# Optimization experiments

Measured on AMD Instinct MI355X. Metric: run time of the kernel, lower is better.

Reference implementation:

```python
import jax, jax.numpy as jnp
import numpy as np

B, N, C, R = 16, 1024, 256, 8
E = 262144
NUM_SUPER = 32
EPS = 1e-5


def _ln(x, g, b):
    mu = jnp.mean(x, axis=-1, keepdims=True)
    var = jnp.var(x, axis=-1, keepdims=True)
    return (x - mu) / jnp.sqrt(var + EPS) * g + b


def setup_inputs() -> dict:
    key = jax.random.key(0)
    ks = jax.random.split(key, 20)

    def w(k, shape, fan_in):
        return (jax.random.normal(k, shape, jnp.float32) / np.sqrt(fan_in)).astype(jnp.float32)

    return dict(
        x=jax.random.normal(ks[0], (B, N, C), jnp.float32),
        batch_edge_index=jax.random.randint(ks[1], (2, E), 0, B * N),
        batch_edge_types=jax.random.randint(ks[2], (E,), 0, R),
        # cross-modal attention
        Wq=w(ks[3], (C, C), C), bq=jnp.zeros((C,), jnp.float32),
        Wk=w(ks[4], (C, C), C), bk=jnp.zeros((C,), jnp.float32),
        Wv=w(ks[5], (C, C), C), bv=jnp.zeros((C,), jnp.float32),
        Wg=w(ks[6], (2 * C, C), 2 * C), bg=jnp.zeros((C,), jnp.float32),
        ln_attn_g=jnp.ones((C,), jnp.float32), ln_attn_b=jnp.zeros((C,), jnp.float32),
        # confidence net
        Wc1=w(ks[7], (C, C // 2), C), bc1=jnp.zeros((C // 2,), jnp.float32),
        Wc2=w(ks[8], (C // 2, 1), C // 2), bc2=jnp.zeros((1,), jnp.float32),
        # feature mixer
        Wm=w(ks[9], (2 * C, C), 2 * C), bm=jnp.zeros((C,), jnp.float32),
        ln1_g=jnp.ones((C,), jnp.float32), ln1_b=jnp.zeros((C,), jnp.float32),
        # RGCN
        W_rel=w(ks[10], (R, C, C), C),
        W_root=w(ks[11], (C, C), C),
        b_rgcn=jnp.zeros((C,), jnp.float32),
        ln2_g=jnp.ones((C,), jnp.float32), ln2_b=jnp.zeros((C,), jnp.float32),
        # super class head
        Wh=w(ks[12], (C, NUM_SUPER), C), bh=jnp.zeros((NUM_SUPER,), jnp.float32),
    )


def reference(x, batch_edge_index, batch_edge_types,
              Wq, bq, Wk, bk, Wv, bv, Wg, bg, ln_attn_g, ln_attn_b,
              Wc1, bc1, Wc2, bc2, Wm, bm, ln1_g, ln1_b,
              W_rel, W_root, b_rgcn, ln2_g, ln2_b, Wh, bh):
    residual = x
    q = x @ Wq + bq
    k = x @ Wk + bk
    v = x @ Wv + bv
    attn = jax.nn.softmax(jnp.einsum('bnc,bmc->bnm', q, k) / jnp.sqrt(jnp.float32(C)), axis=-1)
    out = jnp.einsum('bnm,bmc->bnc', attn, v)
    gate = jax.nn.sigmoid(jnp.concatenate([out, residual], axis=-1) @ Wg + bg)
    validated = _ln(gate * out + (1.0 - gate) * residual, ln_attn_g, ln_attn_b)

    conf = jax.nn.sigmoid(jax.nn.relu(validated @ Wc1 + bc1) @ Wc2 + bc2)  # [B,N,1]
    weighted = validated * conf
    xm = jax.nn.relu(jnp.concatenate([x, weighted], axis=-1) @ Wm + bm)
    xn = _ln(xm, ln1_g, ln1_b).reshape(B * N, C)

    # RGCNConv (PyG defaults: mean aggregation per relation, root weight, bias)
    src, dst = batch_edge_index[0], batch_edge_index[1]
    h = jnp.einsum('nc,rcd->rnd', xn, W_rel)          # [R, B*N, C] relation-transformed nodes
    msg = h[batch_edge_types, src]                    # [E, C] per-edge gather
    seg = dst * R + batch_edge_types                  # (node, relation) segment id
    cnt = jax.ops.segment_sum(jnp.ones((E,), xn.dtype), seg, num_segments=B * N * R)
    msg = msg / jnp.maximum(cnt[seg], 1.0)[:, None]
    agg = jax.ops.segment_sum(msg, dst, num_segments=B * N)
    x_rgcn = agg + xn @ W_root + b_rgcn
    x_rgcn = jax.nn.relu(_ln(x_rgcn.reshape(B, N, C), ln2_g, ln2_b))

    denom = jnp.maximum(conf.sum(axis=1), 1e-8)       # [B,1]
    pooled = (x_rgcn * conf).sum(axis=1) / denom      # [B,C]
    return pooled @ Wh + bh                           # [B, NUM_SUPER]
```

## Files before the change

### kernel.cpp

```cpp
#include <hip/hip_runtime.h>
#include <hip/hip_bf16.h>

#define B_ 16
#define N_ 1024
#define C_ 256
#define R_ 8
#define E_ 262144
#define NS_ 32
#define BN_ (B_*N_)
#define BNC_ (BN_*C_)

typedef __hip_bfloat16 bf16;
typedef __attribute__((ext_vector_type(4))) float f32x4;
typedef __attribute__((ext_vector_type(8))) short bf16x8;

__device__ __forceinline__ float b2f(bf16 x) { return __bfloat162float(x); }
__device__ __forceinline__ bf16  f2b(float x) { return __float2bfloat16(x); }
__device__ __forceinline__ float us2f(unsigned short u) { return __uint_as_float((unsigned)u << 16); }

__device__ __forceinline__ void gload16(const void* g, void* l) {
    auto gp = (const __attribute__((address_space(1))) void*)(unsigned long long)g;
    auto lp = (__attribute__((address_space(3))) void*)(unsigned)(unsigned long long)l;
    __builtin_amdgcn_global_load_lds(gp, lp, 16, 0, 0);
}

template<int ACT>
__global__ __launch_bounds__(256) void gemm_bf16(
    const bf16* __restrict__ A, int lda, long long sA,
    const bf16* __restrict__ Bm, int ldb, long long sB,
    bf16* __restrict__ Cc, int ldc, long long sC,
    const float* __restrict__ bias, const float* __restrict__ bias2,
    const float* __restrict__ bias3, int K)
{
    __shared__ short sbuf[24576];
    const int tid = threadIdx.x;
    const int lane = tid & 63, w = tid >> 6;
    const int wr = w >> 1, wc = w & 1;

    const int gx = gridDim.x;
    const int nwg = gx * gridDim.y;
    int id = blockIdx.y * gx + blockIdx.x;
    if ((nwg & 7) == 0) { const int cpx = nwg >> 3; id = (id & 7) * cpx + (id >> 3); }
    const int bm = (id / gx) * 128, bn = (id % gx) * 128;

    const bf16* Ab = A + (size_t)blockIdx.z * sA;
    const bf16* Bb = Bm + (size_t)blockIdx.z * sB;
    bf16* Cb = Cc + (size_t)blockIdx.z * sC;

    const int rg = lane >> 2;
    const int kswz = ((lane & 3) ^ ((rg >> 1) & 3)) * 8;

    f32x4 acc[4][4];
    const f32x4 zz = {0.f, 0.f, 0.f, 0.f};
    #pragma unroll
    for (int i = 0; i < 4; ++i)
        #pragma unroll
        for (int j = 0; j < 4; ++j) acc[i][j] = zz;

    const int fr = lane & 15;
    const int fm = lane >> 4;
    const int fslot = (fm ^ ((fr >> 1) & 3)) * 8;

    const int NI = K >> 5;

#define STAGE_AB(bi, kk) do {                                                          \
    _Pragma("unroll")                                                                  \
    for (int t_ = 0; t_ < 2; ++t_) {                                                   \
        gload16(Ab + (size_t)(bm + t_*64 + w*16 + rg) * lda + (kk) + kswz,             \
                sbuf + (bi)*4096 + t_*2048 + w*512);                                   \
        gload16(Bb + (size_t)(bn + t_*64 + w*16 + rg) * ldb + (kk) + kswz,             \
                sbuf + 12288 + (bi)*4096 + t_*2048 + w*512);                           \
    } } while (0)

    STAGE_AB(0, 0);
    if (NI > 1) STAGE_AB(1, 32);
    if (NI > 2) STAGE_AB(2, 64);

    int cur = 0;
    for (int i = 0; i < NI; ++i) {
        if (i + 2 < NI)      asm volatile("s_waitcnt vmcnt(8)" ::: "memory");
        else if (i + 1 < NI) asm volatile("s_waitcnt vmcnt(4)" ::: "memory");
        else                 asm volatile("s_waitcnt vmcnt(0)" ::: "memory");
        __builtin_amdgcn_s_barrier();
        __builtin_amdgcn_sched_barrier(0);

        bf16x8 af[4], bfr[4];
        const short* Ac = sbuf + cur * 4096;
        const short* Bc = sbuf + 12288 + cur * 4096;
        #pragma unroll
        for (int ii = 0; ii < 4; ++ii)
            af[ii] = *(const bf16x8*)&Ac[(wr*64 + ii*16 + fr)*32 + fslot];
        #pragma unroll
        for (int jj = 0; jj < 4; ++jj)
            bfr[jj] = *(const bf16x8*)&Bc[(wc*64 + jj*16 + fr)*32 + fslot];

        asm volatile("s_waitcnt lgkmcnt(0)" ::: "memory");
        __builtin_amdgcn_s_barrier();
        __builtin_amdgcn_sched_barrier(0);
        if (i + 3 < NI) STAGE_AB(cur, (i + 3) * 32);

        #pragma unroll
        for (int ii = 0; ii < 4; ++ii)
            #pragma unroll
            for (int jj = 0; jj < 4; ++jj)
                acc[ii][jj] = __builtin_amdgcn_mfma_f32_16x16x32_bf16(af[ii], bfr[jj], acc[ii][jj], 0, 0, 0);
        cur = (cur == 2) ? 0 : cur + 1;
    }
#undef STAGE_AB

    __syncthreads();
    const int er = (lane >> 4) * 4, ec = lane & 15;
    #pragma unroll
    for (int half = 0; half < 2; ++half) {
        if (wr == half) {
            #pragma unroll
            for (int j = 0; j < 4; ++j) {
                const int col = bn + wc*64 + j*16 + ec;
                float bvv = 0.0f;
                if (bias) {
                    const int seg = col >> 8;
                    const float* bp = (seg == 0) ? bias : (seg == 1 ? bias2 : bias3);
                    bvv = bp[col & 255];
                }
                #pragma unroll
                for (int i = 0; i < 4; ++i) {
                    #pragma unroll
                    for (int p = 0; p < 4; ++p) {
                        float val = acc[i][j][p] + bvv;
                        if (ACT == 1) val = fmaxf(val, 0.0f);
                        if (ACT == 2) val = 1.0f / (1.0f + __expf(-val));
                        *(bf16*)&sbuf[(i*16 + er + p)*136 + wc*64 + j*16 + ec] = f2b(val);
                    }
                }
            }
        }
        __syncthreads();
        #pragma unroll
        for (int it = 0; it < 4; ++it) {
            const int ch = tid + it*256;
            const int row = ch >> 4, cp = (ch & 15) * 8;
            *(bf16x8*)&Cb[(size_t)(bm + half*64 + row) * ldc + bn + cp] =
                *(const bf16x8*)&sbuf[row*136 + cp];
        }
        __syncthreads();
    }
}

template<int ACT>
__global__ __launch_bounds__(256) void gemm64_bf16(
    const bf16* __restrict__ A, int lda, long long sA,
    const bf16* __restrict__ Bm, int ldb, long long sB,
    bf16* __restrict__ Cc, int ldc, long long sC,
    const float* __restrict__ bias, int K)
{
    __shared__ short sbuf[16384];
    const int tid = threadIdx.x;
    const int lane = tid & 63, w = tid >> 6;
    const int wr = w >> 1, wc = w & 1;

    const int gx = gridDim.x;
    const int nwg = gx * gridDim.y;
    int id = blockIdx.y * gx + blockIdx.x;
    if ((nwg & 7) == 0) { const int cpx = nwg >> 3; id = (id & 7) * cpx + (id >> 3); }
    const int bm = (id / gx) * 64, bn = (id % gx) * 64;

    const bf16* Ab = A + (size_t)blockIdx.z * sA;
    const bf16* Bb = Bm + (size_t)blockIdx.z * sB;
    bf16* Cb = Cc + (size_t)blockIdx.z * sC;

    const int rg = lane >> 2;
    const int kswz = ((lane & 3) ^ ((rg >> 1) & 3)) * 8;

    f32x4 acc[2][2];
    const f32x4 zz = {0.f, 0.f, 0.f, 0.f};
    #pragma unroll
    for (int i = 0; i < 2; ++i)
        #pragma unroll
        for (int j = 0; j < 2; ++j) acc[i][j] = zz;

    const int fr = lane & 15;
    const int fm = lane >> 4;
    const int fslot = (fm ^ ((fr >> 1) & 3)) * 8;

    const int NI = K >> 5;

#define STAGE64(bi, kk) do {                                                           \
    gload16(Ab + (size_t)(bm + w*16 + rg) * lda + (kk) + kswz,                         \
            sbuf + (bi)*2048 + w*512);                                                 \
    gload16(Bb + (size_t)(bn + w*16 + rg) * ldb + (kk) + kswz,                         \
            sbuf + 8192 + (bi)*2048 + w*512);                                          \
    } while (0)

    STAGE64(0, 0);
    if (NI > 1) STAGE64(1, 32);
    if (NI > 2) STAGE64(2, 64);
    if (NI > 3) STAGE64(3, 96);

    for (int i = 0; i < NI; ++i) {
        const int cur = i & 3;
        if (i + 3 < NI)      asm volatile("s_waitcnt vmcnt(6)" ::: "memory");
        else if (i + 2 < NI) asm volatile("s_waitcnt vmcnt(4)" ::: "memory");
        else if (i + 1 < NI) asm volatile("s_waitcnt vmcnt(2)" ::: "memory");
        else                 asm volatile("s_waitcnt vmcnt(0)" ::: "memory");
        __builtin_amdgcn_s_barrier();
        __builtin_amdgcn_sched_barrier(0);

        bf16x8 af[2], bfr[2];
        const short* Ac = sbuf + cur * 2048;
        const short* Bc = sbuf + 4096*2 + cur * 2048;
        #pragma unroll
        for (int ii = 0; ii < 2; ++ii)
            af[ii] = *(const bf16x8*)&Ac[(wr*32 + ii*16 + fr)*32 + fslot];
        #pragma unroll
        for (int jj = 0; jj < 2; ++jj)
            bfr[jj] = *(const bf16x8*)&Bc[(wc*32 + jj*16 + fr)*32 + fslot];

        asm volatile("s_waitcnt lgkmcnt(0)" ::: "memory");
        __builtin_amdgcn_s_barrier();
        __builtin_amdgcn_sched_barrier(0);
        if (i + 4 < NI) STAGE64(cur, (i + 4) * 32);

        #pragma unroll
        for (int ii = 0; ii < 2; ++ii)
            #pragma unroll
            for (int jj = 0; jj < 2; ++jj)
                acc[ii][jj] = __builtin_amdgcn_mfma_f32_16x16x32_bf16(af[ii], bfr[jj], acc[ii][jj], 0, 0, 0);
    }
#undef STAGE64

    __syncthreads();
    const int er = (lane >> 4) * 4, ec = lane & 15;
    #pragma unroll
    for (int j = 0; j < 2; ++j) {
        const int col = bn + wc*32 + j*16 + ec;
        const float bvv = bias ? bias[col & 255] : 0.0f;
        #pragma unroll
        for (int i = 0; i < 2; ++i) {
            #pragma unroll
            for (int p = 0; p < 4; ++p) {
                float val = acc[i][j][p] + bvv;
                if (ACT == 1) val = fmaxf(val, 0.0f);
                if (ACT == 2) val = 1.0f / (1.0f + __expf(-val));
                *(bf16*)&sbuf[(wr*32 + i*16 + er + p)*72 + wc*32 + j*16 + ec] = f2b(val);
            }
        }
    }
    __syncthreads();
    #pragma unroll
    for (int it = 0; it < 2; ++it) {
        const int ch = tid + it*256;
        const int row = ch >> 3, cp = (ch & 7) * 8;
        *(bf16x8*)&Cb[(size_t)(bm + row) * ldc + bn + cp] =
            *(const bf16x8*)&sbuf[row*72 + cp];
    }
}

__global__ __launch_bounds__(256) void prep_w_k(
    const float* __restrict__ Wq, const float* __restrict__ Wk, const float* __restrict__ Wv,
    const float* __restrict__ Wg, const float* __restrict__ Wm, const float* __restrict__ Wc1,
    const float* __restrict__ Wrel, const float* __restrict__ Wroot, bf16* __restrict__ WT)
{
    int t = blockIdx.x;
    const float* in; bf16* out; int K, Nn;
    if (t < 192)      { int wsel = t >> 6; t &= 63;
                        in = wsel == 0 ? Wq : (wsel == 1 ? Wk : Wv);
                        out = WT + wsel*65536; K = 256; Nn = 256; }
    else if (t < 320) { t -= 192; in = Wg;  out = WT + 196608; K = 512; Nn = 256; }
    else if (t < 448) { t -= 320; in = Wm;  out = WT + 327680; K = 512; Nn = 256; }
    else if (t < 480) { t -= 448; in = Wc1; out = WT + 458752; K = 256; Nn = 128; }
    else if (t < 992) { t -= 480; int r = t >> 6; t &= 63;
                        in = Wrel + (size_t)r*65536; out = WT + 491520 + r*65536; K = 256; Nn = 256; }
    else              { t -= 992; in = Wroot; out = WT + 491520 + 524288; K = 256; Nn = 256; }
    const int tpr = Nn >> 5;
    const int n0 = (t % tpr) * 32, k0 = (t / tpr) * 32;
    __shared__ float tile[32][33];
    const int tx = threadIdx.x & 31, ty = threadIdx.x >> 5;
    #pragma unroll
    for (int i = 0; i < 4; ++i) {
        int r = ty + i*8;
        tile[r][tx] = in[(size_t)(k0 + r) * Nn + n0 + tx];
    }
    __syncthreads();
    #pragma unroll
    for (int i = 0; i < 4; ++i) {
        int r = ty + i*8;
        out[(size_t)(n0 + r) * K + k0 + tx] = f2b(tile[tx][r]);
    }
}

__global__ __launch_bounds__(256) void vtrans_k(
    const bf16* __restrict__ in, bf16* __restrict__ out)
{
    __shared__ float tile[32][33];
    in  += (size_t)blockIdx.z * 786432 + 512;
    out += (size_t)blockIdx.z * 262144;
    const int n0 = blockIdx.x * 32, k0 = blockIdx.y * 32;
    const int tx = threadIdx.x & 31, ty = threadIdx.x >> 5;
    #pragma unroll
    for (int i = 0; i < 4; ++i) {
        int r = ty + i*8;
        tile[r][tx] = b2f(in[(size_t)(k0 + r) * 768 + n0 + tx]);
    }
    __syncthreads();
    #pragma unroll
    for (int i = 0; i < 4; ++i) {
        int r = ty + i*8;
        out[(size_t)(n0 + r) * 1024 + k0 + tx] = f2b(tile[tx][r]);
    }
}

__global__ __launch_bounds__(256) void cvt_x_k(const float* __restrict__ x,
    bf16* __restrict__ xb, bf16* __restrict__ cat1, bf16* __restrict__ cat2)
{
    const int i4 = (blockIdx.x * 256 + threadIdx.x) * 4;
    const float4 xv = *(const float4*)(x + i4);
    bf16 bv[4] = { f2b(xv.x), f2b(xv.y), f2b(xv.z), f2b(xv.w) };
    const ushort4 pack = *(const ushort4*)bv;
    const int row = i4 >> 8, col = i4 & 255;
    *(ushort4*)(xb + i4) = pack;
    *(ushort4*)(cat1 + (size_t)row * 512 + 256 + col) = pack;
    *(ushort4*)(cat2 + (size_t)row * 512 + col) = pack;
}

__global__ __launch_bounds__(256) void softmax_k(bf16* __restrict__ s)
{
    const int row = blockIdx.x, tid = threadIdx.x;
    const int lane = tid & 63, wid = tid >> 6;
    bf16* rp = s + (size_t)row * 1024 + tid * 4;
    __shared__ float red[8];
    const ushort4 sv = *(const ushort4*)rp;
    float v0 = us2f(sv.x) * 0.0625f, v1 = us2f(sv.y) * 0.0625f;
    float v2 = us2f(sv.z) * 0.0625f, v3 = us2f(sv.w) * 0.0625f;
    float m = fmaxf(fmaxf(v0, v1), fmaxf(v2, v3));
    #pragma unroll
    for (int o = 32; o >= 1; o >>= 1) m = fmaxf(m, __shfl_xor(m, o));
    if (lane == 0) red[wid] = m;
    __syncthreads();
    const float mx = fmaxf(fmaxf(red[0], red[1]), fmaxf(red[2], red[3]));
    float e0 = __expf(v0 - mx), e1 = __expf(v1 - mx), e2 = __expf(v2 - mx), e3 = __expf(v3 - mx);
    float sm = e0 + e1 + e2 + e3;
    #pragma unroll
    for (int o = 32; o >= 1; o >>= 1) sm += __shfl_xor(sm, o);
    if (lane == 0) red[4 + wid] = sm;
    __syncthreads();
    const float inv = 1.0f / (red[4] + red[5] + red[6] + red[7]);
    bf16 ov[4] = { f2b(e0 * inv), f2b(e1 * inv), f2b(e2 * inv), f2b(e3 * inv) };
    *(ushort4*)rp = *(const ushort4*)ov;
}

template<int RELU>
__global__ __launch_bounds__(256) void ln_k(
    const bf16* __restrict__ in, bf16* __restrict__ out,
    const float* __restrict__ g, const float* __restrict__ bta)
{
    const int node = blockIdx.x * 4 + (threadIdx.x >> 6);
    const int lane = threadIdx.x & 63;
    const ushort4 iv = *(const ushort4*)(in + (size_t)node * 256 + lane * 4);
    float v0 = us2f(iv.x), v1 = us2f(iv.y), v2 = us2f(iv.z), v3 = us2f(iv.w);
    float s  = v0 + v1 + v2 + v3;
    float sq = v0*v0 + v1*v1 + v2*v2 + v3*v3;
    #pragma unroll
    for (int o = 32; o >= 1; o >>= 1) { s += __shfl_xor(s, o); sq += __shfl_xor(sq, o); }
    const float mean = s * (1.0f / 256.0f);
    const float var  = sq * (1.0f / 256.0f) - mean * mean;
    const float rs = rsqrtf(var + 1e-5f);
    const float4 gv = *(const float4*)(g + lane * 4);
    const float4 bv = *(const float4*)(bta + lane * 4);
    float y0 = (v0 - mean) * rs * gv.x + bv.x;
    float y1 = (v1 - mean) * rs * gv.y + bv.y;
    float y2 = (v2 - mean) * rs * gv.z + bv.z;
    float y3 = (v3 - mean) * rs * gv.w + bv.w;
    if (RELU) { y0 = fmaxf(y0, 0.f); y1 = fmaxf(y1, 0.f); y2 = fmaxf(y2, 0.f); y3 = fmaxf(y3, 0.f); }
    bf16 ov[4] = { f2b(y0), f2b(y1), f2b(y2), f2b(y3) };
    *(ushort4*)(out + (size_t)node * 256 + lane * 4) = *(const ushort4*)ov;
}

__global__ __launch_bounds__(256) void blend_ln_k(
    const bf16* __restrict__ gate, const bf16* __restrict__ cat1,
    const bf16* __restrict__ xb, bf16* __restrict__ valid,
    const float* __restrict__ g, const float* __restrict__ bta)
{
    const int node = blockIdx.x * 4 + (threadIdx.x >> 6);
    const int lane = threadIdx.x & 63;
    const ushort4 gt4 = *(const ushort4*)(gate + (size_t)node * 256 + lane * 4);
    const ushort4 ao4 = *(const ushort4*)(cat1 + (size_t)node * 512 + lane * 4);
    const ushort4 xv4 = *(const ushort4*)(xb + (size_t)node * 256 + lane * 4);
    float g0 = us2f(gt4.x), g1 = us2f(gt4.y), g2 = us2f(gt4.z), g3 = us2f(gt4.w);
    float v0 = g0 * us2f(ao4.x) + (1.f - g0) * us2f(xv4.x);
    float v1 = g1 * us2f(ao4.y) + (1.f - g1) * us2f(xv4.y);
    float v2 = g2 * us2f(ao4.z) + (1.f - g2) * us2f(xv4.z);
    float v3 = g3 * us2f(ao4.w) + (1.f - g3) * us2f(xv4.w);
    float s  = v0 + v1 + v2 + v3;
    float sq = v0*v0 + v1*v1 + v2*v2 + v3*v3;
    #pragma unroll
    for (int o = 32; o >= 1; o >>= 1) { s += __shfl_xor(s, o); sq += __shfl_xor(sq, o); }
    const float mean = s * (1.0f / 256.0f);
    const float var  = sq * (1.0f / 256.0f) - mean * mean;
    const float rs = rsqrtf(var + 1e-5f);
    const float4 gv = *(const float4*)(g + lane * 4);
    const float4 bv = *(const float4*)(bta + lane * 4);
    bf16 ov[4] = { f2b((v0 - mean) * rs * gv.x + bv.x), f2b((v1 - mean) * rs * gv.y + bv.y),
                   f2b((v2 - mean) * rs * gv.z + bv.z), f2b((v3 - mean) * rs * gv.w + bv.w) };
    *(ushort4*)(valid + (size_t)node * 256 + lane * 4) = *(const ushort4*)ov;
}

__global__ __launch_bounds__(256) void conf_w_k(
    const bf16* __restrict__ t1, const float* __restrict__ Wc2, const float* __restrict__ bc2,
    const bf16* __restrict__ valid, float* __restrict__ conf, bf16* __restrict__ cat2)
{
    const int node = blockIdx.x * 4 + (threadIdx.x >> 6);
    const int lane = threadIdx.x & 63;
    float a = b2f(t1[(size_t)node * 128 + lane]) * Wc2[lane]
            + b2f(t1[(size_t)node * 128 + 64 + lane]) * Wc2[64 + lane];
    #pragma unroll
    for (int o = 32; o >= 1; o >>= 1) a += __shfl_xor(a, o);
    const float c = 1.0f / (1.0f + __expf(-(a + bc2[0])));
    if (lane == 0) conf[node] = c;
    const ushort4 vv = *(const ushort4*)(valid + (size_t)node * 256 + lane * 4);
    bf16 ov[4] = { f2b(us2f(vv.x) * c), f2b(us2f(vv.y) * c), f2b(us2f(vv.z) * c), f2b(us2f(vv.w) * c) };
    *(ushort4*)(cat2 + (size_t)node * 512 + 256 + lane * 4) = *(const ushort4*)ov;
}

__global__ __launch_bounds__(256) void count2_k(
    const int* __restrict__ dst, const int* __restrict__ et,
    int* __restrict__ deg, int* __restrict__ cnt8)
{
    const int e = blockIdx.x * 256 + threadIdx.x;
    if (e < E_) {
        const int d = dst[e];
        atomicAdd(&deg[d], 1);
        atomicAdd(&cnt8[d * 8 + et[e]], 1);
    }
}

__global__ __launch_bounds__(256) void scan_k(
    const int* __restrict__ deg, int* __restrict__ rowptr, int* __restrict__ cursor)
{
    __shared__ int part[256];
    const int tid = threadIdx.x;
    const int base = tid * 64;
    int s = 0;
    for (int i = 0; i < 64; ++i) s += deg[base + i];
    part[tid] = s; __syncthreads();
    for (int off = 1; off < 256; off <<= 1) {
        int t = (tid >= off) ? part[tid - off] : 0;
        __syncthreads();
        part[tid] += t;
        __syncthreads();
    }
    int run = (tid == 0) ? 0 : part[tid - 1];
    for (int i = 0; i < 64; ++i) {
        rowptr[base + i] = run;
        cursor[base + i] = run;
        run += deg[base + i];
    }
    if (tid == 255) rowptr[BN_] = run;
}

__global__ __launch_bounds__(256) void fill_k(
    const int* __restrict__ src, const int* __restrict__ dst, const int* __restrict__ et,
    int* __restrict__ cursor, int* __restrict__ elist)
{
    const int e = blockIdx.x * 256 + threadIdx.x;
    if (e < E_) {
        const int pos = atomicAdd(&cursor[dst[e]], 1);
        elist[pos] = src[e] | (et[e] << 16);
    }
}

__global__ __launch_bounds__(256) void gather_ln_k(
    const int* __restrict__ rowptr, const int* __restrict__ elist,
    const bf16* __restrict__ h, const int* __restrict__ cnt8,
    const float* __restrict__ brg,
    const float* __restrict__ g, const float* __restrict__ bta,
    bf16* __restrict__ xr)
{
    const int node = blockIdx.x * 4 + (threadIdx.x >> 6);
    const int lane = threadIdx.x & 63;
    const int e0 = rowptr[node], e1 = rowptr[node + 1];
    float invc[8];
    #pragma unroll
    for (int r = 0; r < 8; ++r)
        invc[r] = 1.0f / fmaxf((float)cnt8[node * 8 + r], 1.0f);
    float a0 = 0.f, a1 = 0.f, a2 = 0.f, a3 = 0.f;
    int e = e0;
    for (; e + 3 < e1; e += 4) {
        const int p0 = elist[e], p1 = elist[e+1], p2 = elist[e+2], p3 = elist[e+3];
        const float w0 = invc[p0 >> 16], w1 = invc[p1 >> 16];
        const float w2 = invc[p2 >> 16], w3 = invc[p3 >> 16];
        const ushort4 h0 = *(const ushort4*)(h + (size_t)(p0 & 0xffff) * 2304 + (p0 >> 16) * 256 + lane * 4);
        const ushort4 h1 = *(const ushort4*)(h + (size_t)(p1 & 0xffff) * 2304 + (p1 >> 16) * 256 + lane * 4);
        const ushort4 h2 = *(const ushort4*)(h + (size_t)(p2 & 0xffff) * 2304 + (p2 >> 16) * 256 + lane * 4);
        const ushort4 h3 = *(const ushort4*)(h + (size_t)(p3 & 0xffff) * 2304 + (p3 >> 16) * 256 + lane * 4);
        a0 += w0 * us2f(h0.x) + w1 * us2f(h1.x) + w2 * us2f(h2.x) + w3 * us2f(h3.x);
        a1 += w0 * us2f(h0.y) + w1 * us2f(h1.y) + w2 * us2f(h2.y) + w3 * us2f(h3.y);
        a2 += w0 * us2f(h0.z) + w1 * us2f(h1.z) + w2 * us2f(h2.z) + w3 * us2f(h3.z);
        a3 += w0 * us2f(h0.w) + w1 * us2f(h1.w) + w2 * us2f(h2.w) + w3 * us2f(h3.w);
    }
    for (; e < e1; ++e) {
        const int pe = elist[e];
        const float wgt = invc[pe >> 16];
        const ushort4 hv = *(const ushort4*)(h + (size_t)(pe & 0xffff) * 2304 + (pe >> 16) * 256 + lane * 4);
        a0 += wgt * us2f(hv.x); a1 += wgt * us2f(hv.y);
        a2 += wgt * us2f(hv.z); a3 += wgt * us2f(hv.w);
    }
    const ushort4 rv = *(const ushort4*)(h + (size_t)node * 2304 + 2048 + lane * 4);
    const float4 bg4 = *(const float4*)(brg + lane * 4);
    const float v0 = a0 + us2f(rv.x) + bg4.x, v1 = a1 + us2f(rv.y) + bg4.y;
    const float v2 = a2 + us2f(rv.z) + bg4.z, v3 = a3 + us2f(rv.w) + bg4.w;
    float s  = v0 + v1 + v2 + v3;
    float sq = v0*v0 + v1*v1 + v2*v2 + v3*v3;
    #pragma unroll
    for (int m = 32; m >= 1; m >>= 1) { s += __shfl_xor(s, m); sq += __shfl_xor(sq, m); }
    const float mean = s * (1.0f / 256.0f);
    const float var  = sq * (1.0f / 256.0f) - mean * mean;
    const float rs = rsqrtf(var + 1e-5f);
    const float4 gv = *(const float4*)(g + lane * 4);
    const float4 bv = *(const float4*)(bta + lane * 4);
    bf16 tb[4] = { f2b(fmaxf((v0 - mean) * rs * gv.x + bv.x, 0.f)),
                   f2b(fmaxf((v1 - mean) * rs * gv.y + bv.y, 0.f)),
                   f2b(fmaxf((v2 - mean) * rs * gv.z + bv.z, 0.f)),
                   f2b(fmaxf((v3 - mean) * rs * gv.w + bv.w, 0.f)) };
    *(ushort4*)(xr + (size_t)node * 256 + lane * 4) = *(const ushort4*)tb;
}

__global__ __launch_bounds__(256) void pool1_k(
    const bf16* __restrict__ xr, const float* __restrict__ conf, float* __restrict__ partial)
{
    const int b = blockIdx.x, chunk = blockIdx.y, c = threadIdx.x;
    float acc = 0.0f;
    for (int n = 0; n < 64; ++n) {
        const int node = b * 1024 + chunk * 64 + n;
        acc += conf[node] * b2f(xr[(size_t)node * 256 + c]);
    }
    partial[(size_t)(b * 16 + chunk) * 256 + c] = acc;
}

__global__ __launch_bounds__(256) void pool2_k(
    const float* __restrict__ partial, const float* __restrict__ conf,
    const float* __restrict__ Wh, const float* __restrict__ bh, float* __restrict__ out)
{
    const int b = blockIdx.x, tid = threadIdx.x;
    __shared__ float red[256];
    __shared__ float pooled[256];
    float pc = 0.0f;
    for (int ch = 0; ch < 16; ++ch) pc += partial[(size_t)(b * 16 + ch) * 256 + tid];
    float s = conf[b * 1024 + tid] + conf[b * 1024 + 256 + tid]
            + conf[b * 1024 + 512 + tid] + conf[b * 1024 + 768 + tid];
    red[tid] = s; __syncthreads();
    for (int st = 128; st > 0; st >>= 1) { if (tid < st) red[tid] += red[tid + st]; __syncthreads(); }
    const float denom = fmaxf(red[0], 1e-8f);
    pooled[tid] = pc / denom;
    __syncthreads();
    if (tid < NS_) {
        float o = bh[tid];
        for (int c = 0; c < 256; ++c) o += pooled[c] * Wh[c * NS_ + tid];
        out[b * NS_ + tid] = o;
    }
}

extern "C" void kernel_launch(void* const* d_in, const int* in_sizes, int n_in,
                              void* d_out, int out_size, void* d_ws, size_t ws_size,
                              hipStream_t stream) {
    const float* x    = (const float*)d_in[0];
    const int*   ei   = (const int*)d_in[1];
    const int*   et   = (const int*)d_in[2];
    const float* Wq   = (const float*)d_in[3];  const float* bq  = (const float*)d_in[4];
    const float* Wk   = (const float*)d_in[5];  const float* bk  = (const float*)d_in[6];
    const float* Wv   = (const float*)d_in[7];  const float* bv  = (const float*)d_in[8];
    const float* Wg   = (const float*)d_in[9];  const float* bg  = (const float*)d_in[10];
    const float* lag  = (const float*)d_in[11]; const float* lab = (const float*)d_in[12];
    const float* Wc1  = (const float*)d_in[13]; const float* bc1 = (const float*)d_in[14];
    const float* Wc2  = (const float*)d_in[15]; const float* bc2 = (const float*)d_in[16];
    const float* Wm   = (const float*)d_in[17]; const float* bm  = (const float*)d_in[18];
    const float* l1g  = (const float*)d_in[19]; const float* l1b = (const float*)d_in[20];
    const float* Wrel = (const float*)d_in[21]; const float* Wroot = (const float*)d_in[22];
    const float* brg  = (const float*)d_in[23];
    const float* l2g  = (const float*)d_in[24]; const float* l2b = (const float*)d_in[25];
    const float* Wh   = (const float*)d_in[26]; const float* bh  = (const float*)d_in[27];
    const int* esrc = ei;
    const int* edst = ei + E_;

    char* w8 = (char*)d_ws;
    bf16*  qkv   = (bf16*)(w8 + 0);
    bf16*  hbuf  = (bf16*)(w8 + 0);
    bf16*  sP    = (bf16*)(w8 + 25165824);
    bf16*  cat1  = (bf16*)(w8 + 58720256);
    bf16*  cat2  = (bf16*)(w8 + 75497472);
    bf16*  gate  = (bf16*)(w8 + 92274688);
    bf16*  valid = (bf16*)(w8 + 100663296);
    bf16*  t1    = (bf16*)(w8 + 109051904);
    bf16*  xm    = (bf16*)(w8 + 113246208);
    bf16*  xb    = (bf16*)(w8 + 121634816);
    bf16*  xn    = (bf16*)(w8 + 130023424);
    bf16*  vtb   = (bf16*)(w8 + 138412032);
    bf16*  xr    = (bf16*)(w8 + 146800640);
    float* conf  = (float*)(w8 + 155189248);
    float* part  = (float*)(w8 + 155254784);
    bf16*  WT    = (bf16*)(w8 + 155516928);
    int*  deg    = (int*)(w8 + 157679616);
    int*  cnt8i  = (int*)(w8 + 157745152);
    int*  rowptr = (int*)(w8 + 158269440);
    int*  cursor = (int*)(w8 + 158335232);
    int*  elist  = (int*)(w8 + 158400768);
    bf16* WqkvT = WT;
    bf16* WgT   = WT + 196608;
    bf16* WmT   = WT + 327680;
    bf16* Wc1T  = WT + 458752;
    bf16* WBIG  = WT + 491520;
    float* outp = (float*)d_out;

    dim3 blk(256);

    prep_w_k<<<1056, blk, 0, stream>>>(Wq, Wk, Wv, Wg, Wm, Wc1, Wrel, Wroot, WT);
    cvt_x_k<<<BNC_ / 1024, blk, 0, stream>>>(x, xb, cat1, cat2);
    hipMemsetAsync(deg, 0, 589824, stream);
    count2_k<<<E_ / 256, blk, 0, stream>>>(edst, et, deg, cnt8i);
    scan_k<<<1, blk, 0, stream>>>(deg, rowptr, cursor);
    fill_k<<<E_ / 256, blk, 0, stream>>>(esrc, edst, et, cursor, elist);

    gemm_bf16<0><<<dim3(6, 128, 1), blk, 0, stream>>>(
        xb, 256, 0, WqkvT, 256, 0, qkv, 768, 0, bq, bk, bv, 256);
    vtrans_k<<<dim3(8, 32, 16), blk, 0, stream>>>(qkv, vtb);

    gemm_bf16<0><<<dim3(8, 8, 16), blk, 0, stream>>>(
        qkv, 768, 786432, qkv + 256, 768, 786432, sP, 1024, 1048576, nullptr, nullptr, nullptr, 256);
    softmax_k<<<BN_, blk, 0, stream>>>(sP);
    gemm_bf16<0><<<dim3(2, 8, 16), blk, 0, stream>>>(
        sP, 1024, 1048576, vtb, 1024, 262144, cat1, 512, 524288, nullptr, nullptr, nullptr, 1024);

    gemm64_bf16<2><<<dim3(4, 256, 1), blk, 0, stream>>>(
        cat1, 512, 0, WgT, 512, 0, gate, 256, 0, bg, 512);
    blend_ln_k<<<BN_ / 4, blk, 0, stream>>>(gate, cat1, xb, valid, lag, lab);

    gemm64_bf16<1><<<dim3(2, 256, 1), blk, 0, stream>>>(
        valid, 256, 0, Wc1T, 256, 0, t1, 128, 0, bc1, 256);
    conf_w_k<<<BN_ / 4, blk, 0, stream>>>(t1, Wc2, bc2, valid, conf, cat2);

    gemm64_bf16<1><<<dim3(4, 256, 1), blk, 0, stream>>>(
        cat2, 512, 0, WmT, 512, 0, xm, 256, 0, bm, 512);
    ln_k<0><<<BN_ / 4, blk, 0, stream>>>(xm, xn, l1g, l1b);

    gemm_bf16<0><<<dim3(18, 128, 1), blk, 0, stream>>>(
        xn, 256, 0, WBIG, 256, 0, hbuf, 2304, 0, nullptr, nullptr, nullptr, 256);
    gather_ln_k<<<BN_ / 4, blk, 0, stream>>>(rowptr, elist, hbuf, cnt8i, brg, l2g, l2b, xr);

    pool1_k<<<dim3(B_, 16), blk, 0, stream>>>(xr, conf, part);
    pool2_k<<<B_, blk, 0, stream>>>(part, conf, Wh, bh, outp);
}
```

Before: 261.2 us.

## Aggregate-then-transform RGCN via per-relation mean gather and single K=2304 GEMM

Reorders the RGCN so neighbour features are first mean-aggregated per (node, relation) from xn into a concatenated [BN, 2304] buffer, then multiplied once by the stacked W_rel/W_root weights in a K=2304 GEMM. Edge sorting now uses (dst, relation) buckets, the weight prep writes the stacked transposed layout, and a separate ln_k handles the bias-added LayerNorm+ReLU. This removes the wide 2304-column h GEMM output and the gathers into it, at the cost of a long-K GEMM with few output tiles. The QK^T score GEMM is also switched to the 64-tile kernel.

New measurement: 323.3 us. 23.8% more time.

```diff
diff --git a/kernel.cpp b/kernel.cpp
--- a/kernel.cpp
+++ b/kernel.cpp
@@ -207,7 +207,7 @@
 
         bf16x8 af[2], bfr[2];
         const short* Ac = sbuf + cur * 2048;
-        const short* Bc = sbuf + 4096*2 + cur * 2048;
+        const short* Bc = sbuf + 8192 + cur * 2048;
         #pragma unroll
         for (int ii = 0; ii < 2; ++ii)
             af[ii] = *(const bf16x8*)&Ac[(wr*32 + ii*16 + fr)*32 + fslot];
@@ -261,16 +261,16 @@
     const float* __restrict__ Wrel, const float* __restrict__ Wroot, bf16* __restrict__ WT)
 {
     int t = blockIdx.x;
-    const float* in; bf16* out; int K, Nn;
+    const float* in; bf16* out; int Nn, ldout, kofs;
     if (t < 192)      { int wsel = t >> 6; t &= 63;
                         in = wsel == 0 ? Wq : (wsel == 1 ? Wk : Wv);
-                        out = WT + wsel*65536; K = 256; Nn = 256; }
-    else if (t < 320) { t -= 192; in = Wg;  out = WT + 196608; K = 512; Nn = 256; }
-    else if (t < 448) { t -= 320; in = Wm;  out = WT + 327680; K = 512; Nn = 256; }
-    else if (t < 480) { t -= 448; in = Wc1; out = WT + 458752; K = 256; Nn = 128; }
+                        out = WT + wsel*65536; Nn = 256; ldout = 256; kofs = 0; }
+    else if (t < 320) { t -= 192; in = Wg;  out = WT + 196608; Nn = 256; ldout = 512; kofs = 0; }
+    else if (t < 448) { t -= 320; in = Wm;  out = WT + 327680; Nn = 256; ldout = 512; kofs = 0; }
+    else if (t < 480) { t -= 448; in = Wc1; out = WT + 458752; Nn = 128; ldout = 256; kofs = 0; }
     else if (t < 992) { t -= 480; int r = t >> 6; t &= 63;
-                        in = Wrel + (size_t)r*65536; out = WT + 491520 + r*65536; K = 256; Nn = 256; }
-    else              { t -= 992; in = Wroot; out = WT + 491520 + 524288; K = 256; Nn = 256; }
+                        in = Wrel + (size_t)r*65536; out = WT + 491520; Nn = 256; ldout = 2304; kofs = r*256; }
+    else              { t -= 992; in = Wroot; out = WT + 491520; Nn = 256; ldout = 2304; kofs = 2048; }
     const int tpr = Nn >> 5;
     const int n0 = (t % tpr) * 32, k0 = (t / tpr) * 32;
     __shared__ float tile[32][33];
@@ -284,7 +284,7 @@
     #pragma unroll
     for (int i = 0; i < 4; ++i) {
         int r = ty + i*8;
-        out[(size_t)(n0 + r) * K + k0 + tx] = f2b(tile[tx][r]);
+        out[(size_t)(n0 + r) * ldout + kofs + k0 + tx] = f2b(tile[tx][r]);
     }
 }
 
@@ -421,26 +421,21 @@
     *(ushort4*)(cat2 + (size_t)node * 512 + 256 + lane * 4) = *(const ushort4*)ov;
 }
 
-__global__ __launch_bounds__(256) void count2_k(
-    const int* __restrict__ dst, const int* __restrict__ et,
-    int* __restrict__ deg, int* __restrict__ cnt8)
+__global__ __launch_bounds__(256) void count8_k(
+    const int* __restrict__ dst, const int* __restrict__ et, int* __restrict__ cnt8)
 {
     const int e = blockIdx.x * 256 + threadIdx.x;
-    if (e < E_) {
-        const int d = dst[e];
-        atomicAdd(&deg[d], 1);
-        atomicAdd(&cnt8[d * 8 + et[e]], 1);
-    }
-}
-
-__global__ __launch_bounds__(256) void scan_k(
-    const int* __restrict__ deg, int* __restrict__ rowptr, int* __restrict__ cursor)
+    if (e < E_) atomicAdd(&cnt8[dst[e] * 8 + et[e]], 1);
+}
+
+__global__ __launch_bounds__(256) void scan8_k(
+    const int* __restrict__ cnt8, int* __restrict__ rowptr8, int* __restrict__ cursor8)
 {
     __shared__ int part[256];
     const int tid = threadIdx.x;
-    const int base = tid * 64;
+    const int base = tid * 512;
     int s = 0;
-    for (int i = 0; i < 64; ++i) s += deg[base + i];
+    for (int i = 0; i < 512; ++i) s += cnt8[base + i];
     part[tid] = s; __syncthreads();
     for (int off = 1; off < 256; off <<= 1) {
         int t = (tid >= off) ? part[tid - off] : 0;
@@ -449,79 +444,56 @@
         __syncthreads();
     }
     int run = (tid == 0) ? 0 : part[tid - 1];
-    for (int i = 0; i < 64; ++i) {
-        rowptr[base + i] = run;
-        cursor[base + i] = run;
-        run += deg[base + i];
-    }
-    if (tid == 255) rowptr[BN_] = run;
-}
-
-__global__ __launch_bounds__(256) void fill_k(
+    for (int i = 0; i < 512; ++i) {
+        rowptr8[base + i] = run;
+        cursor8[base + i] = run;
+        run += cnt8[base + i];
+    }
+    if (tid == 255) rowptr8[BN_ * 8] = run;
+}
+
+__global__ __launch_bounds__(256) void fill8_k(
     const int* __restrict__ src, const int* __restrict__ dst, const int* __restrict__ et,
-    int* __restrict__ cursor, int* __restrict__ elist)
+    int* __restrict__ cursor8, int* __restrict__ elist)
 {
     const int e = blockIdx.x * 256 + threadIdx.x;
     if (e < E_) {
-        const int pos = atomicAdd(&cursor[dst[e]], 1);
-        elist[pos] = src[e] | (et[e] << 16);
-    }
-}
-
-__global__ __launch_bounds__(256) void gather_ln_k(
-    const int* __restrict__ rowptr, const int* __restrict__ elist,
-    const bf16* __restrict__ h, const int* __restrict__ cnt8,
-    const float* __restrict__ brg,
-    const float* __restrict__ g, const float* __restrict__ bta,
-    bf16* __restrict__ xr)
+        const int pos = atomicAdd(&cursor8[dst[e] * 8 + et[e]], 1);
+        elist[pos] = src[e];
+    }
+}
+
+__global__ __launch_bounds__(256) void gather_sum_k(
+    const int* __restrict__ rowptr8, const int* __restrict__ elist,
+    const bf16* __restrict__ xn, bf16* __restrict__ S)
 {
     const int node = blockIdx.x * 4 + (threadIdx.x >> 6);
     const int lane = threadIdx.x & 63;
-    const int e0 = rowptr[node], e1 = rowptr[node + 1];
-    float invc[8];
-    #pragma unroll
-    for (int r = 0; r < 8; ++r)
-        invc[r] = 1.0f / fmaxf((float)cnt8[node * 8 + r], 1.0f);
-    float a0 = 0.f, a1 = 0.f, a2 = 0.f, a3 = 0.f;
-    int e = e0;
-    for (; e + 3 < e1; e += 4) {
-        const int p0 = elist[e], p1 = elist[e+1], p2 = elist[e+2], p3 = elist[e+3];
-        const float w0 = invc[p0 >> 16], w1 = invc[p1 >> 16];
-        const float w2 = invc[p2 >> 16], w3 = invc[p3 >> 16];
-        const ushort4 h0 = *(const ushort4*)(h + (size_t)(p0 & 0xffff) * 2304 + (p0 >> 16) * 256 + lane * 4);
-        const ushort4 h1 = *(const ushort4*)(h + (size_t)(p1 & 0xffff) * 2304 + (p1 >> 16) * 256 + lane * 4);
-        const ushort4 h2 = *(const ushort4*)(h + (size_t)(p2 & 0xffff) * 2304 + (p2 >> 16) * 256 + lane * 4);
-        const ushort4 h3 = *(const ushort4*)(h + (size_t)(p3 & 0xffff) * 2304 + (p3 >> 16) * 256 + lane * 4);
-        a0 += w0 * us2f(h0.x) + w1 * us2f(h1.x) + w2 * us2f(h2.x) + w3 * us2f(h3.x);
-        a1 += w0 * us2f(h0.y) + w1 * us2f(h1.y) + w2 * us2f(h2.y) + w3 * us2f(h3.y);
-        a2 += w0 * us2f(h0.z) + w1 * us2f(h1.z) + w2 * us2f(h2.z) + w3 * us2f(h3.z);
-        a3 += w0 * us2f(h0.w) + w1 * us2f(h1.w) + w2 * us2f(h2.w) + w3 * us2f(h3.w);
-    }
-    for (; e < e1; ++e) {
-        const int pe = elist[e];
-        const float wgt = invc[pe >> 16];
-        const ushort4 hv = *(const ushort4*)(h + (size_t)(pe & 0xffff) * 2304 + (pe >> 16) * 256 + lane * 4);
-        a0 += wgt * us2f(hv.x); a1 += wgt * us2f(hv.y);
-        a2 += wgt * us2f(hv.z); a3 += wgt * us2f(hv.w);
-    }
-    const ushort4 rv = *(const ushort4*)(h + (size_t)node * 2304 + 2048 + lane * 4);
-    const float4 bg4 = *(const float4*)(brg + lane * 4);
-    const float v0 = a0 + us2f(rv.x) + bg4.x, v1 = a1 + us2f(rv.y) + bg4.y;
-    const float v2 = a2 + us2f(rv.z) + bg4.z, v3 = a3 + us2f(rv.w) + bg4.w;
-    float s  = v0 + v1 + v2 + v3;
-    float sq = v0*v0 + v1*v1 + v2*v2 + v3*v3;
-    #pragma unroll
-    for (int m = 32; m >= 1; m >>= 1) { s += __shfl_xor(s, m); sq += __shfl_xor(sq, m); }
-    const float mean = s * (1.0f / 256.0f);
-    const float var  = sq * (1.0f / 256.0f) - mean * mean;
-    const float rs = rsqrtf(var + 1e-5f);
-    const float4 gv = *(const float4*)(g + lane * 4);
-    const float4 bv = *(const float4*)(bta + lane * 4);
-    bf16 tb[4] = { f2b(fmaxf((v0 - mean) * rs * gv.x + bv.x, 0.f)),
-                   f2b(fmaxf((v1 - mean) * rs * gv.y + bv.y, 0.f)),
-                   f2b(fmaxf((v2 - mean) * rs * gv.z + bv.z, 0.f)),
-                   f2b(fmaxf((v3 - mean) * rs * gv.w + bv.w, 0.f)) };
-    *(ushort4*)(xr + (size_t)node * 256 + lane * 4) = *(const ushort4*)tb;
+    bf16* Srow = S + (size_t)node * 2304;
+    *(ushort4*)(Srow + 2048 + lane * 4) = *(const ushort4*)(xn + (size_t)node * 256 + lane * 4);
+    const int base = node * 8;
+    #pragma unroll
+    for (int r = 0; r < 8; ++r) {
+        const int e0 = rowptr8[base + r], e1 = rowptr8[base + r + 1];
+        float a0 = 0.f, a1 = 0.f, a2 = 0.f, a3 = 0.f;
+        int e = e0;
+        for (; e + 1 < e1; e += 2) {
+            const int s0 = elist[e], s1 = elist[e + 1];
+            const ushort4 h0 = *(const ushort4*)(xn + (size_t)s0 * 256 + lane * 4);
+            const ushort4 h1 = *(const ushort4*)(xn + (size_t)s1 * 256 + lane * 4);
+            a0 += us2f(h0.x) + us2f(h1.x);
+            a1 += us2f(h0.y) + us2f(h1.y);
+            a2 += us2f(h0.z) + us2f(h1.z);
+            a3 += us2f(h0.w) + us2f(h1.w);
+        }
+        if (e < e1) {
+            const ushort4 hv = *(const ushort4*)(xn + (size_t)elist[e] * 256 + lane * 4);
+            a0 += us2f(hv.x); a1 += us2f(hv.y); a2 += us2f(hv.z); a3 += us2f(hv.w);
+        }
+        const float inv = 1.0f / fmaxf((float)(e1 - e0), 1.0f);
+        bf16 ov[4] = { f2b(a0 * inv), f2b(a1 * inv), f2b(a2 * inv), f2b(a3 * inv) };
+        *(ushort4*)(Srow + r * 256 + lane * 4) = *(const ushort4*)ov;
+    }
 }
 
 __global__ __launch_bounds__(256) void pool1_k(
@@ -583,7 +555,7 @@
 
     char* w8 = (char*)d_ws;
     bf16*  qkv   = (bf16*)(w8 + 0);
-    bf16*  hbuf  = (bf16*)(w8 + 0);
+    bf16*  Sbig  = (bf16*)(w8 + 0);
     bf16*  sP    = (bf16*)(w8 + 25165824);
     bf16*  cat1  = (bf16*)(w8 + 58720256);
     bf16*  cat2  = (bf16*)(w8 + 75497472);
@@ -598,33 +570,33 @@
     float* conf  = (float*)(w8 + 155189248);
     float* part  = (float*)(w8 + 155254784);
     bf16*  WT    = (bf16*)(w8 + 155516928);
-    int*  deg    = (int*)(w8 + 157679616);
-    int*  cnt8i  = (int*)(w8 + 157745152);
-    int*  rowptr = (int*)(w8 + 158269440);
-    int*  cursor = (int*)(w8 + 158335232);
-    int*  elist  = (int*)(w8 + 158400768);
+    int*  cnt8i   = (int*)(w8 + 157679616);
+    int*  rowptr8 = (int*)(w8 + 158203904);
+    int*  cursor8 = (int*)(w8 + 158728448);
+    int*  elist   = (int*)(w8 + 159252736);
     bf16* WqkvT = WT;
     bf16* WgT   = WT + 196608;
     bf16* WmT   = WT + 327680;
     bf16* Wc1T  = WT + 458752;
-    bf16* WBIG  = WT + 491520;
+    bf16* WB2   = WT + 491520;
+    bf16* aggb  = gate;
     float* outp = (float*)d_out;
 
     dim3 blk(256);
 
     prep_w_k<<<1056, blk, 0, stream>>>(Wq, Wk, Wv, Wg, Wm, Wc1, Wrel, Wroot, WT);
     cvt_x_k<<<BNC_ / 1024, blk, 0, stream>>>(x, xb, cat1, cat2);
-    hipMemsetAsync(deg, 0, 589824, stream);
-    count2_k<<<E_ / 256, blk, 0, stream>>>(edst, et, deg, cnt8i);
-    scan_k<<<1, blk, 0, stream>>>(deg, rowptr, cursor);
-    fill_k<<<E_ / 256, blk, 0, stream>>>(esrc, edst, et, cursor, elist);
+    hipMemsetAsync(cnt8i, 0, (size_t)BN_ * 8 * sizeof(int), stream);
+    count8_k<<<E_ / 256, blk, 0, stream>>>(edst, et, cnt8i);
+    scan8_k<<<1, blk, 0, stream>>>(cnt8i, rowptr8, cursor8);
+    fill8_k<<<E_ / 256, blk, 0, stream>>>(esrc, edst, et, cursor8, elist);
 
     gemm_bf16<0><<<dim3(6, 128, 1), blk, 0, stream>>>(
         xb, 256, 0, WqkvT, 256, 0, qkv, 768, 0, bq, bk, bv, 256);
     vtrans_k<<<dim3(8, 32, 16), blk, 0, stream>>>(qkv, vtb);
 
-    gemm_bf16<0><<<dim3(8, 8, 16), blk, 0, stream>>>(
-        qkv, 768, 786432, qkv + 256, 768, 786432, sP, 1024, 1048576, nullptr, nullptr, nullptr, 256);
+    gemm64_bf16<0><<<dim3(16, 16, 16), blk, 0, stream>>>(
+        qkv, 768, 786432, qkv + 256, 768, 786432, sP, 1024, 1048576, nullptr, 256);
     softmax_k<<<BN_, blk, 0, stream>>>(sP);
     gemm_bf16<0><<<dim3(2, 8, 16), blk, 0, stream>>>(
         sP, 1024, 1048576, vtb, 1024, 262144, cat1, 512, 524288, nullptr, nullptr, nullptr, 1024);
@@ -641,9 +613,10 @@
         cat2, 512, 0, WmT, 512, 0, xm, 256, 0, bm, 512);
     ln_k<0><<<BN_ / 4, blk, 0, stream>>>(xm, xn, l1g, l1b);
 
-    gemm_bf16<0><<<dim3(18, 128, 1), blk, 0, stream>>>(
-        xn, 256, 0, WBIG, 256, 0, hbuf, 2304, 0, nullptr, nullptr, nullptr, 256);
-    gather_ln_k<<<BN_ / 4, blk, 0, stream>>>(rowptr, elist, hbuf, cnt8i, brg, l2g, l2b, xr);
+    gather_sum_k<<<BN_ / 4, blk, 0, stream>>>(rowptr8, elist, xn, Sbig);
+    gemm_bf16<0><<<dim3(2, 128, 1), blk, 0, stream>>>(
+        Sbig, 2304, 0, WB2, 2304, 0, aggb, 256, 0, brg, nullptr, nullptr, 2304);
+    ln_k<1><<<BN_ / 4, blk, 0, stream>>>(aggb, xr, l2g, l2b);
 
     pool1_k<<<dim3(B_, 16), blk, 0, stream>>>(xr, conf, part);
     pool2_k<<<B_, blk, 0, stream>>>(part, conf, Wh, bh, outp);
```
